# Performance work log

Hardware: AMD Instinct MI355X
Metric: run time of the kernel (lower is better)

Reference implementation:

```python
import jax, jax.numpy as jnp
import numpy as np

NUM_EXPERTS = 8
TOP_K = 2
HIDDEN = 1024
INTER = 1408


def setup_inputs() -> dict:
    key = jax.random.key(0)
    k0, k1, k2, k3, k4 = jax.random.split(key, 5)
    B, S = 2, 2048
    d_scale = HIDDEN ** -0.5
    i_scale = INTER ** -0.5
    return {
        "hidden_states": jax.random.normal(k0, (B, S, HIDDEN), jnp.float32),
        # nn.Linear(hidden, num_experts, bias=False): weight (E, d)
        "gate_w": jax.random.normal(k1, (NUM_EXPERTS, HIDDEN), jnp.float32) * d_scale,
        # per-expert SwiGLU weights, nn.Linear convention (out, in)
        "gate_proj": jax.random.normal(k2, (NUM_EXPERTS, INTER, HIDDEN), jnp.float32) * d_scale,
        "up_proj": jax.random.normal(k3, (NUM_EXPERTS, INTER, HIDDEN), jnp.float32) * d_scale,
        "down_proj": jax.random.normal(k4, (NUM_EXPERTS, HIDDEN, INTER), jnp.float32) * i_scale,
    }


def reference(hidden_states, gate_w, gate_proj, up_proj, down_proj):
    B, S, D = hidden_states.shape
    x = hidden_states.reshape(-1, D)  # (T, d)
    T = x.shape[0]

    # gate linear -> router logits (T, E)
    router_logits = x @ gate_w.T

    # TopKRouter: softmax in fp32 over all experts, top-k, optional renorm
    probs = jax.nn.softmax(router_logits.astype(jnp.float32), axis=-1)
    routing_weights, selected_experts = jax.lax.top_k(probs, TOP_K)  # (T, k)
    routing_weights = routing_weights / routing_weights.sum(axis=-1, keepdims=True)  # norm_topk_prob
    routing_weights = routing_weights.astype(x.dtype)

    # combine weights per (token, expert): scatter top-k weights into dense (T, E)
    combine = jnp.zeros((T, NUM_EXPERTS), x.dtype).at[
        jnp.arange(T)[:, None], selected_experts
    ].add(routing_weights)

    # per-expert SwiGLU FFN, weighted combine (loop over small fixed expert set)
    out = jnp.zeros_like(x)
    for e in range(NUM_EXPERTS):
        h = jax.nn.silu(x @ gate_proj[e].T) * (x @ up_proj[e].T)  # (T, i)
        out = out + combine[:, e : e + 1] * (h @ down_proj[e].T)  # (T, d)

    return out.reshape(B, S, D), router_logits
```

## Files before the change

### kernel.cpp

```cpp
#include <hip/hip_runtime.h>
#include <hip/hip_bf16.h>
#include <stdint.h>

#define T_TOK 4096
#define DH 1024
#define DI 1408
#define NE 8
#define TOPK 2
#define PADROWS 9216

typedef short s16x8 __attribute__((ext_vector_type(8)));
typedef float f32x4 __attribute__((ext_vector_type(4)));

__device__ inline unsigned f2bf(float f) {
    __hip_bfloat16 h = __float2bfloat16(f);
    return (unsigned)*(unsigned short*)&h;
}
__device__ inline float bf2f(unsigned short u) {
    return __uint_as_float(((unsigned)u) << 16);
}

#define GLDS(src, dst) __builtin_amdgcn_global_load_lds( \
    (const __attribute__((address_space(1))) void*)(src), \
    (__attribute__((address_space(3))) void*)(dst), 16, 0, 0)

#define SBAR()  __builtin_amdgcn_s_barrier()
#define SCHED() __builtin_amdgcn_sched_barrier(0)

__global__ __launch_bounds__(256) void cvt3_kernel(const float* __restrict__ s0,
        const float* __restrict__ s1, const float* __restrict__ s2,
        uint4* __restrict__ t0, uint4* __restrict__ t1, uint4* __restrict__ t2, int n8) {
    int i = blockIdx.x * blockDim.x + threadIdx.x;
    int stride = gridDim.x * blockDim.x;
    const float4* f0 = (const float4*)s0;
    const float4* f1 = (const float4*)s1;
    const float4* f2 = (const float4*)s2;
    for (; i < n8; i += stride) {
        float4 a0 = f0[2 * i], b0 = f0[2 * i + 1];
        float4 a1 = f1[2 * i], b1 = f1[2 * i + 1];
        float4 a2 = f2[2 * i], b2 = f2[2 * i + 1];
        uint4 o0, o1, o2;
        o0.x = f2bf(a0.x) | (f2bf(a0.y) << 16); o0.y = f2bf(a0.z) | (f2bf(a0.w) << 16);
        o0.z = f2bf(b0.x) | (f2bf(b0.y) << 16); o0.w = f2bf(b0.z) | (f2bf(b0.w) << 16);
        o1.x = f2bf(a1.x) | (f2bf(a1.y) << 16); o1.y = f2bf(a1.z) | (f2bf(a1.w) << 16);
        o1.z = f2bf(b1.x) | (f2bf(b1.y) << 16); o1.w = f2bf(b1.z) | (f2bf(b1.w) << 16);
        o2.x = f2bf(a2.x) | (f2bf(a2.y) << 16); o2.y = f2bf(a2.z) | (f2bf(a2.w) << 16);
        o2.z = f2bf(b2.x) | (f2bf(b2.y) << 16); o2.w = f2bf(b2.z) | (f2bf(b2.w) << 16);
        t0[i] = o0; t1[i] = o1; t2[i] = o2;
    }
}

__global__ __launch_bounds__(256) void router_kernel(const float* __restrict__ x,
                              const float* __restrict__ gw,
                              float* __restrict__ logits_out,
                              int* __restrict__ tokE, float* __restrict__ tokW,
                              unsigned short* __restrict__ xb) {
    int wave = threadIdx.x >> 6;
    int lane = threadIdx.x & 63;
    int t = blockIdx.x * 4 + wave;
    const float4* xr = (const float4*)(x + (size_t)t * DH);

    float acc[NE];
#pragma unroll
    for (int e = 0; e < NE; ++e) acc[e] = 0.f;

#pragma unroll
    for (int i = 0; i < 4; ++i) {
        float4 xv = xr[lane + i * 64];
#pragma unroll
        for (int e = 0; e < NE; ++e) {
            float4 g = ((const float4*)(gw + (size_t)e * DH))[lane + i * 64];
            acc[e] += xv.x * g.x + xv.y * g.y + xv.z * g.z + xv.w * g.w;
        }
        uint2 o;
        o.x = f2bf(xv.x) | (f2bf(xv.y) << 16);
        o.y = f2bf(xv.z) | (f2bf(xv.w) << 16);
        *(uint2*)(xb + (size_t)t * DH + (lane + i * 64) * 4) = o;
    }
#pragma unroll
    for (int e = 0; e < NE; ++e) {
#pragma unroll
        for (int off = 32; off > 0; off >>= 1) acc[e] += __shfl_xor(acc[e], off, 64);
    }
    if (lane == 0) {
        float mx = acc[0];
#pragma unroll
        for (int e = 1; e < NE; ++e) mx = fmaxf(mx, acc[e]);
        float p[NE]; float s = 0.f;
#pragma unroll
        for (int e = 0; e < NE; ++e) { p[e] = expf(acc[e] - mx); s += p[e]; }
        float inv = 1.f / s;
#pragma unroll
        for (int e = 0; e < NE; ++e) p[e] *= inv;
        int i0 = 0, i1 = -1; float p0 = -1.f, p1 = -1.f;
#pragma unroll
        for (int e = 0; e < NE; ++e) {
            float v = p[e];
            if (v > p0) { p1 = p0; i1 = i0; p0 = v; i0 = e; }
            else if (v > p1) { p1 = v; i1 = e; }
        }
        float wsum = p0 + p1;
#pragma unroll
        for (int e = 0; e < NE; ++e) logits_out[(size_t)t * NE + e] = acc[e];
        tokE[2 * t]     = i0;  tokE[2 * t + 1] = i1;
        tokW[2 * t]     = p0 / wsum;  tokW[2 * t + 1] = p1 / wsum;
    }
}

__global__ __launch_bounds__(1024) void histscatter_kernel(const int* __restrict__ tokE,
        int* __restrict__ countsG, int* __restrict__ padOffG,
        int* __restrict__ assignTok, int* __restrict__ tokSlot) {
    __shared__ int wc[16][NE];
    __shared__ int padOff[NE + 1];
    __shared__ int cursor[NE];
    int tid = threadIdx.x, wave = tid >> 6, lane = tid & 63;

    int cnt[NE];
#pragma unroll
    for (int e = 0; e < NE; ++e) cnt[e] = 0;
    for (int i = tid; i < T_TOK * TOPK; i += 1024) {
        int v = tokE[i];
#pragma unroll
        for (int e = 0; e < NE; ++e)
            cnt[e] += (int)__popcll(__ballot(v == e));
    }
    for (int i = tid; i < PADROWS; i += 1024) assignTok[i] = 0;
    if (lane == 0) {
#pragma unroll
        for (int e = 0; e < NE; ++e) wc[wave][e] = cnt[e];
    }
    __syncthreads();
    if (tid == 0) {
        int r = 0;
        for (int e = 0; e < NE; ++e) {
            int c = 0;
            for (int w = 0; w < 16; ++w) c += wc[w][e];
            countsG[e] = c;
            padOff[e] = r;
            padOffG[e] = r;
            cursor[e] = 0;
            r += ((c + 127) >> 7) << 7;
        }
        padOff[NE] = r;
        padOffG[NE] = r;
    }
    __syncthreads();

    unsigned long long lmask = (1ull << lane) - 1ull;
    for (int i = tid; i < T_TOK * TOPK; i += 1024) {
        int e = tokE[i];
#pragma unroll
        for (int ex = 0; ex < NE; ++ex) {
            unsigned long long m = __ballot(e == ex);
            if (e == ex) {
                int rank = (int)__popcll(m & lmask);
                int leader = __ffsll((long long)m) - 1;
                int b = 0;
                if (rank == 0) b = atomicAdd(&cursor[ex], (int)__popcll(m));
                b = __shfl(b, leader, 64);
                int slot = padOff[ex] + b + rank;
                assignTok[slot] = i >> 1;
                tokSlot[i] = slot;
            }
        }
    }
}

__global__ __launch_bounds__(512) void gemmA_kernel(
        const unsigned short* __restrict__ xb,
        const unsigned short* __restrict__ gpb, const unsigned short* __restrict__ upb,
        const int* __restrict__ padOff, const int* __restrict__ assignTok,
        unsigned short* __restrict__ h) {
    int bid = blockIdx.x;
    int nid = (bid & 7) * 99 + (bid >> 3);
    int colblk = nid / 72, rowblk = nid - colblk * 72;
    int pr0 = rowblk * 128;
    int n0 = colblk * 128;
    int e = -1;
#pragma unroll
    for (int i = 0; i < NE; ++i)
        if (pr0 >= padOff[i] && pr0 < padOff[i + 1]) e = i;
    if (e < 0) return;

    __shared__ unsigned short As[3][128 * 32];
    __shared__ unsigned short Bgs[3][128 * 32];
    __shared__ unsigned short Bus[3][128 * 32];

    int tid = threadIdx.x;
    int lane = tid & 63;
    int w = tid >> 6;
    int wm = (w >> 2) * 64;
    int wn = (w & 3) * 32;

    int srow = w * 16 + (lane >> 2);
    int aslot = (((lane & 3) ^ ((lane >> 3) & 3)) << 3);
    int tok = assignTok[pr0 + srow];
    const unsigned short* a0   = xb  + (size_t)tok * DH + aslot;
    const unsigned short* gsrc = gpb + ((size_t)e * DI + n0 + srow) * DH + aslot;
    const unsigned short* usrc = upb + ((size_t)e * DI + n0 + srow) * DH + aslot;
    int sdst = w * 512;

    int rq = (((lane >> 4) ^ ((lane >> 1) & 3)) << 3);

    f32x4 accG[4][2], accU[4][2];
#pragma unroll
    for (int i = 0; i < 4; ++i)
#pragma unroll
        for (int j = 0; j < 2; ++j) {
            accG[i][j] = (f32x4){0.f, 0.f, 0.f, 0.f};
            accU[i][j] = (f32x4){0.f, 0.f, 0.f, 0.f};
        }

#define STAGE_A(buf, k0) do { \
    GLDS(a0 + (k0),   &As[buf][sdst]); \
    GLDS(gsrc + (k0), &Bgs[buf][sdst]); \
    GLDS(usrc + (k0), &Bus[buf][sdst]); \
    } while (0)

#define KCOMP_A(cur, VMS) do { \
    asm volatile("s_waitcnt vmcnt(" VMS ")" ::: "memory"); \
    SBAR(); SCHED(); \
    s16x8 af[4], bgf[2], bu2[2]; \
    _Pragma("unroll") \
    for (int i = 0; i < 4; ++i) \
        af[i] = *(const s16x8*)&As[cur][(wm + 16 * i + (lane & 15)) * 32 + rq]; \
    _Pragma("unroll") \
    for (int j = 0; j < 2; ++j) { \
        bgf[j] = *(const s16x8*)&Bgs[cur][(wn + 16 * j + (lane & 15)) * 32 + rq]; \
        bu2[j] = *(const s16x8*)&Bus[cur][(wn + 16 * j + (lane & 15)) * 32 + rq]; \
    } \
    asm volatile("s_waitcnt lgkmcnt(0)" ::: "memory"); \
    SCHED(); \
    SBAR(); \
    SCHED(); \
    _Pragma("unroll") \
    for (int i = 0; i < 4; ++i) \
        _Pragma("unroll") \
        for (int j = 0; j < 2; ++j) { \
            accG[i][j] = __builtin_amdgcn_mfma_f32_16x16x32_bf16(af[i], bgf[j], accG[i][j], 0, 0, 0); \
            accU[i][j] = __builtin_amdgcn_mfma_f32_16x16x32_bf16(af[i], bu2[j], accU[i][j], 0, 0, 0); \
        } \
    } while (0)

    STAGE_A(0, 0);
    STAGE_A(1, 32);
    int bs = 2, bc = 0;
    for (int ks = 0; ks < 30; ++ks) {
        STAGE_A(bs, (ks + 2) * 32);
        KCOMP_A(bc, "6");
        bs = (bs == 2) ? 0 : bs + 1;
        bc = (bc == 2) ? 0 : bc + 1;
    }
    KCOMP_A(0, "3");
    KCOMP_A(1, "0");
#undef STAGE_A
#undef KCOMP_A

#pragma unroll
    for (int i = 0; i < 4; ++i) {
        int rowb = pr0 + wm + 16 * i + ((lane >> 4) << 2);
#pragma unroll
        for (int j = 0; j < 2; ++j) {
            int col = n0 + wn + 16 * j + (lane & 15);
#pragma unroll
            for (int r = 0; r < 4; ++r) {
                float g = accG[i][j][r], u = accU[i][j][r];
                float val = (g / (1.f + __expf(-g))) * u;
                h[(size_t)(rowb + r) * DI + col] = (unsigned short)f2bf(val);
            }
        }
    }
}

__global__ __launch_bounds__(256) void gemmB_kernel(
        const unsigned short* __restrict__ h,
        const unsigned short* __restrict__ dpb,
        const int* __restrict__ padOff, const int* __restrict__ counts,
        unsigned short* __restrict__ outP) {
    int bid = blockIdx.x;
    int nid = (bid & 7) * 72 + (bid >> 3);
    int colblk = nid / 72, rowblk = nid - colblk * 72;
    int pr0 = rowblk * 128;
    int n0 = colblk * 128;
    int e = -1, base = 0;
#pragma unroll
    for (int i = 0; i < NE; ++i)
        if (pr0 >= padOff[i] && pr0 < padOff[i + 1]) { e = i; base = padOff[i]; }
    if (e < 0) return;
    int cnt = counts[e];

    __shared__ unsigned short As[3][128 * 32];
    __shared__ unsigned short Bs[3][128 * 32];

    int tid = threadIdx.x;
    int lane = tid & 63;
    int w = tid >> 6;
    int wm = (w >> 1) * 64;
    int wn = (w & 1) * 64;

    int srow = w * 32 + (lane >> 2);
    int aslot = (((lane & 3) ^ ((lane >> 3) & 3)) << 3);
    const unsigned short* a0   = h   + (size_t)(pr0 + srow) * DI + aslot;
    const unsigned short* a1   = h   + (size_t)(pr0 + srow + 16) * DI + aslot;
    const unsigned short* b0   = dpb + ((size_t)e * DH + n0 + srow) * DI + aslot;
    const unsigned short* b1   = dpb + ((size_t)e * DH + n0 + srow + 16) * DI + aslot;
    int sdst = w * 1024;

    int rq = (((lane >> 4) ^ ((lane >> 1) & 3)) << 3);

    f32x4 acc[4][4];
#pragma unroll
    for (int i = 0; i < 4; ++i)
#pragma unroll
        for (int j = 0; j < 4; ++j) acc[i][j] = (f32x4){0.f, 0.f, 0.f, 0.f};

#define STAGE_B(buf, k0) do { \
    GLDS(a0 + (k0), &As[buf][sdst]); \
    GLDS(a1 + (k0), &As[buf][sdst + 512]); \
    GLDS(b0 + (k0), &Bs[buf][sdst]); \
    GLDS(b1 + (k0), &Bs[buf][sdst + 512]); \
    } while (0)

#define KCOMP_B(cur, VMS) do { \
    asm volatile("s_waitcnt vmcnt(" VMS ")" ::: "memory"); \
    SBAR(); SCHED(); \
    s16x8 af[4], bf[4]; \
    _Pragma("unroll") \
    for (int i = 0; i < 4; ++i) \
        af[i] = *(const s16x8*)&As[cur][(wm + 16 * i + (lane & 15)) * 32 + rq]; \
    _Pragma("unroll") \
    for (int j = 0; j < 4; ++j) \
        bf[j] = *(const s16x8*)&Bs[cur][(wn + 16 * j + (lane & 15)) * 32 + rq]; \
    asm volatile("s_waitcnt lgkmcnt(0)" ::: "memory"); \
    SCHED(); \
    SBAR(); \
    SCHED(); \
    _Pragma("unroll") \
    for (int i = 0; i < 4; ++i) \
        _Pragma("unroll") \
        for (int j = 0; j < 4; ++j) \
            acc[i][j] = __builtin_amdgcn_mfma_f32_16x16x32_bf16(af[i], bf[j], acc[i][j], 0, 0, 0); \
    } while (0)

    STAGE_B(0, 0);
    STAGE_B(1, 32);
    int bs = 2, bc = 0;
    for (int ks = 0; ks < 42; ++ks) {
        STAGE_B(bs, (ks + 2) * 32);
        KCOMP_B(bc, "8");
        bs = (bs == 2) ? 0 : bs + 1;
        bc = (bc == 2) ? 0 : bc + 1;
    }
    KCOMP_B(0, "4");
    KCOMP_B(1, "0");
#undef STAGE_B
#undef KCOMP_B

#pragma unroll
    for (int i = 0; i < 4; ++i) {
        int rowb = pr0 + wm + 16 * i + ((lane >> 4) << 2);
#pragma unroll
        for (int r = 0; r < 4; ++r) {
            int prow = rowb + r;
            if (prow - base < cnt) {
#pragma unroll
                for (int j = 0; j < 4; ++j) {
                    int col = n0 + wn + 16 * j + (lane & 15);
                    outP[(size_t)prow * DH + col] = (unsigned short)f2bf(acc[i][j][r]);
                }
            }
        }
    }
}

__global__ __launch_bounds__(256) void combine_kernel(const unsigned short* __restrict__ outP,
        const int* __restrict__ tokSlot, const float* __restrict__ tokW,
        float* __restrict__ out) {
    int t = blockIdx.x;
    int c = threadIdx.x * 4;
    int s0 = tokSlot[2 * t], s1 = tokSlot[2 * t + 1];
    float w0 = tokW[2 * t], w1 = tokW[2 * t + 1];
    ushort4 a = *(const ushort4*)(outP + (size_t)s0 * DH + c);
    ushort4 b = *(const ushort4*)(outP + (size_t)s1 * DH + c);
    float4 o;
    o.x = w0 * bf2f(a.x) + w1 * bf2f(b.x);
    o.y = w0 * bf2f(a.y) + w1 * bf2f(b.y);
    o.z = w0 * bf2f(a.z) + w1 * bf2f(b.z);
    o.w = w0 * bf2f(a.w) + w1 * bf2f(b.w);
    *(float4*)(out + (size_t)t * DH + c) = o;
}

extern "C" void kernel_launch(void* const* d_in, const int* in_sizes, int n_in,
                              void* d_out, int out_size, void* d_ws, size_t ws_size,
                              hipStream_t stream) {
    const float* x  = (const float*)d_in[0];
    const float* gw = (const float*)d_in[1];
    const float* gp = (const float*)d_in[2];
    const float* up = (const float*)d_in[3];
    const float* dp = (const float*)d_in[4];
    float* out = (float*)d_out;
    float* logits = out + (size_t)T_TOK * DH;

    char* ws = (char*)d_ws;
    int*   counts    = (int*)(ws + 0);
    int*   padOff    = (int*)(ws + 128);
    int*   tokE      = (int*)(ws + 4096);
    float* tokW      = (float*)(ws + 36864);
    int*   tokSlot   = (int*)(ws + 69632);
    int*   assignTok = (int*)(ws + 102400);
    unsigned short* xb   = (unsigned short*)(ws + 147456);
    unsigned short* gpb  = (unsigned short*)(ws + 8536064);
    unsigned short* upb  = (unsigned short*)(ws + 31604736);
    unsigned short* dpb  = (unsigned short*)(ws + 54673408);
    unsigned short* h    = (unsigned short*)(ws + 77742080);
    unsigned short* outP = (unsigned short*)(ws + 8536064);

    const int NW8 = NE * DI * DH / 8;
    cvt3_kernel<<<2048, 256, 0, stream>>>(gp, up, dp, (uint4*)gpb, (uint4*)upb, (uint4*)dpb, NW8);

    router_kernel<<<T_TOK / 4, 256, 0, stream>>>(x, gw, logits, tokE, tokW, xb);
    histscatter_kernel<<<1, 1024, 0, stream>>>(tokE, counts, padOff, assignTok, tokSlot);

    gemmA_kernel<<<dim3((DI / 128) * (PADROWS / 128)), 512, 0, stream>>>(xb, gpb, upb, padOff, assignTok, h);
    gemmB_kernel<<<(DH / 128) * (PADROWS / 128), 256, 0, stream>>>(h, dpb, padOff, counts, outP);
    combine_kernel<<<T_TOK, 256, 0, stream>>>(outP, tokSlot, tokW, out);
}
```

Baseline: 185.1 us.

## Fuse weighted combine into down-projection GEMM epilogue via atomic adds

```diff
diff --git a/kernel.cpp b/kernel.cpp
--- a/kernel.cpp
+++ b/kernel.cpp
@@ -11,14 +11,13 @@
 
 typedef short s16x8 __attribute__((ext_vector_type(8)));
 typedef float f32x4 __attribute__((ext_vector_type(4)));
+typedef float f32x4v __attribute__((ext_vector_type(4)));
+typedef unsigned u32x4v __attribute__((ext_vector_type(4)));
 
 __device__ inline unsigned f2bf(float f) {
     __hip_bfloat16 h = __float2bfloat16(f);
     return (unsigned)*(unsigned short*)&h;
 }
-__device__ inline float bf2f(unsigned short u) {
-    return __uint_as_float(((unsigned)u) << 16);
-}
 
 #define GLDS(src, dst) __builtin_amdgcn_global_load_lds( \
     (const __attribute__((address_space(1))) void*)(src), \
@@ -29,24 +28,30 @@
 
 __global__ __launch_bounds__(256) void cvt3_kernel(const float* __restrict__ s0,
         const float* __restrict__ s1, const float* __restrict__ s2,
-        uint4* __restrict__ t0, uint4* __restrict__ t1, uint4* __restrict__ t2, int n8) {
+        unsigned* __restrict__ t0, unsigned* __restrict__ t1,
+        unsigned* __restrict__ t2, int n8) {
     int i = blockIdx.x * blockDim.x + threadIdx.x;
     int stride = gridDim.x * blockDim.x;
-    const float4* f0 = (const float4*)s0;
-    const float4* f1 = (const float4*)s1;
-    const float4* f2 = (const float4*)s2;
+    const f32x4v* f0 = (const f32x4v*)s0;
+    const f32x4v* f1 = (const f32x4v*)s1;
+    const f32x4v* f2 = (const f32x4v*)s2;
     for (; i < n8; i += stride) {
-        float4 a0 = f0[2 * i], b0 = f0[2 * i + 1];
-        float4 a1 = f1[2 * i], b1 = f1[2 * i + 1];
-        float4 a2 = f2[2 * i], b2 = f2[2 * i + 1];
-        uint4 o0, o1, o2;
+        f32x4v a0 = __builtin_nontemporal_load(&f0[2 * i]);
+        f32x4v b0 = __builtin_nontemporal_load(&f0[2 * i + 1]);
+        f32x4v a1 = __builtin_nontemporal_load(&f1[2 * i]);
+        f32x4v b1 = __builtin_nontemporal_load(&f1[2 * i + 1]);
+        f32x4v a2 = __builtin_nontemporal_load(&f2[2 * i]);
+        f32x4v b2 = __builtin_nontemporal_load(&f2[2 * i + 1]);
+        u32x4v o0, o1, o2;
         o0.x = f2bf(a0.x) | (f2bf(a0.y) << 16); o0.y = f2bf(a0.z) | (f2bf(a0.w) << 16);
         o0.z = f2bf(b0.x) | (f2bf(b0.y) << 16); o0.w = f2bf(b0.z) | (f2bf(b0.w) << 16);
         o1.x = f2bf(a1.x) | (f2bf(a1.y) << 16); o1.y = f2bf(a1.z) | (f2bf(a1.w) << 16);
         o1.z = f2bf(b1.x) | (f2bf(b1.y) << 16); o1.w = f2bf(b1.z) | (f2bf(b1.w) << 16);
         o2.x = f2bf(a2.x) | (f2bf(a2.y) << 16); o2.y = f2bf(a2.z) | (f2bf(a2.w) << 16);
         o2.z = f2bf(b2.x) | (f2bf(b2.y) << 16); o2.w = f2bf(b2.z) | (f2bf(b2.w) << 16);
-        t0[i] = o0; t1[i] = o1; t2[i] = o2;
+        __builtin_nontemporal_store(o0, (u32x4v*)&t0[4 * i]);
+        __builtin_nontemporal_store(o1, (u32x4v*)&t1[4 * i]);
+        __builtin_nontemporal_store(o2, (u32x4v*)&t2[4 * i]);
     }
 }
 
@@ -108,8 +113,9 @@
 }
 
 __global__ __launch_bounds__(1024) void histscatter_kernel(const int* __restrict__ tokE,
+        const float* __restrict__ tokW,
         int* __restrict__ countsG, int* __restrict__ padOffG,
-        int* __restrict__ assignTok, int* __restrict__ tokSlot) {
+        int* __restrict__ assignTok, float* __restrict__ assignW) {
     __shared__ int wc[16][NE];
     __shared__ int padOff[NE + 1];
     __shared__ int cursor[NE];
@@ -160,7 +166,7 @@
                 b = __shfl(b, leader, 64);
                 int slot = padOff[ex] + b + rank;
                 assignTok[slot] = i >> 1;
-                tokSlot[i] = slot;
+                assignW[slot] = tokW[i];
             }
         }
     }
@@ -276,7 +282,8 @@
         const unsigned short* __restrict__ h,
         const unsigned short* __restrict__ dpb,
         const int* __restrict__ padOff, const int* __restrict__ counts,
-        unsigned short* __restrict__ outP) {
+        const int* __restrict__ assignTok, const float* __restrict__ assignW,
+        float* __restrict__ out) {
     int bid = blockIdx.x;
     int nid = (bid & 7) * 72 + (bid >> 3);
     int colblk = nid / 72, rowblk = nid - colblk * 72;
@@ -363,31 +370,17 @@
         for (int r = 0; r < 4; ++r) {
             int prow = rowb + r;
             if (prow - base < cnt) {
+                int tok = assignTok[prow];
+                float wgt = assignW[prow];
+                float* orow = out + (size_t)tok * DH;
 #pragma unroll
                 for (int j = 0; j < 4; ++j) {
                     int col = n0 + wn + 16 * j + (lane & 15);
-                    outP[(size_t)prow * DH + col] = (unsigned short)f2bf(acc[i][j][r]);
+                    atomicAdd(&orow[col], wgt * acc[i][j][r]);
                 }
             }
         }
     }
-}
-
-__global__ __launch_bounds__(256) void combine_kernel(const unsigned short* __restrict__ outP,
-        const int* __restrict__ tokSlot, const float* __restrict__ tokW,
-        float* __restrict__ out) {
-    int t = blockIdx.x;
-    int c = threadIdx.x * 4;
-    int s0 = tokSlot[2 * t], s1 = tokSlot[2 * t + 1];
-    float w0 = tokW[2 * t], w1 = tokW[2 * t + 1];
-    ushort4 a = *(const ushort4*)(outP + (size_t)s0 * DH + c);
-    ushort4 b = *(const ushort4*)(outP + (size_t)s1 * DH + c);
-    float4 o;
-    o.x = w0 * bf2f(a.x) + w1 * bf2f(b.x);
-    o.y = w0 * bf2f(a.y) + w1 * bf2f(b.y);
-    o.z = w0 * bf2f(a.z) + w1 * bf2f(b.z);
-    o.w = w0 * bf2f(a.w) + w1 * bf2f(b.w);
-    *(float4*)(out + (size_t)t * DH + c) = o;
 }
 
 extern "C" void kernel_launch(void* const* d_in, const int* in_sizes, int n_in,
@@ -406,22 +399,23 @@
     int*   padOff    = (int*)(ws + 128);
     int*   tokE      = (int*)(ws + 4096);
     float* tokW      = (float*)(ws + 36864);
-    int*   tokSlot   = (int*)(ws + 69632);
-    int*   assignTok = (int*)(ws + 102400);
+    float* assignW   = (float*)(ws + 69632);
+    int*   assignTok = (int*)(ws + 106496);
     unsigned short* xb   = (unsigned short*)(ws + 147456);
     unsigned short* gpb  = (unsigned short*)(ws + 8536064);
     unsigned short* upb  = (unsigned short*)(ws + 31604736);
     unsigned short* dpb  = (unsigned short*)(ws + 54673408);
     unsigned short* h    = (unsigned short*)(ws + 77742080);
-    unsigned short* outP = (unsigned short*)(ws + 8536064);
+
+    hipMemsetAsync(d_out, 0, (size_t)T_TOK * DH * sizeof(float), stream);
 
     const int NW8 = NE * DI * DH / 8;
-    cvt3_kernel<<<2048, 256, 0, stream>>>(gp, up, dp, (uint4*)gpb, (uint4*)upb, (uint4*)dpb, NW8);
+    cvt3_kernel<<<2048, 256, 0, stream>>>(gp, up, dp,
+                                          (unsigned*)gpb, (unsigned*)upb, (unsigned*)dpb, NW8);
 
     router_kernel<<<T_TOK / 4, 256, 0, stream>>>(x, gw, logits, tokE, tokW, xb);
-    histscatter_kernel<<<1, 1024, 0, stream>>>(tokE, counts, padOff, assignTok, tokSlot);
+    histscatter_kernel<<<1, 1024, 0, stream>>>(tokE, tokW, counts, padOff, assignTok, assignW);
 
     gemmA_kernel<<<dim3((DI / 128) * (PADROWS / 128)), 512, 0, stream>>>(xb, gpb, upb, padOff, assignTok, h);
-    gemmB_kernel<<<(DH / 128) * (PADROWS / 128), 256, 0, stream>>>(h, dpb, padOff, counts, outP);
-    combine_kernel<<<T_TOK, 256, 0, stream>>>(outP, tokSlot, tokW, out);
-}
+    gemmB_kernel<<<(DH / 128) * (PADROWS / 128), 256, 0, stream>>>(h, dpb, padOff, counts, assignTok, assignW, out);
+}
```

Measured after the change: 225.1 us. +21.6%, slower.
